# Performance work log

Hardware: AMD Instinct MI355X
Metric: run time of the kernel (lower is better)

The kernel has to match this reference:

```python
import jax, jax.numpy as jnp
import numpy as np

L, H, C, HS, V, BS = 4, 4, 1024, 256, 32000, 1024  # layers, heads, n_embd, head_size, vocab, block_size
B, T = 4, 1024
EPS = 1e-5

def _ln(x, g, b):
    mu = jnp.mean(x, axis=-1, keepdims=True)
    var = jnp.mean((x - mu) ** 2, axis=-1, keepdims=True)
    return (x - mu) / jnp.sqrt(var + EPS) * g + b

def setup_inputs() -> dict:
    key = jax.random.key(0)
    ks = iter(jax.random.split(key, 32))
    s = 0.02
    inp = {
        'idx': jax.random.randint(next(ks), (B, T), 0, V),
        'tok_emb': jax.random.normal(next(ks), (V, C), jnp.float32) * s,
        'pos_emb': jax.random.normal(next(ks), (BS, C), jnp.float32) * s,
        'wq': jax.random.normal(next(ks), (L, H, C, HS), jnp.float32) * s,
        'wk': jax.random.normal(next(ks), (L, H, C, HS), jnp.float32) * s,
        'wv': jax.random.normal(next(ks), (L, H, C, HS), jnp.float32) * s,
        'proj_w': jax.random.normal(next(ks), (L, C, C), jnp.float32) * s,
        'proj_b': jnp.zeros((L, C), jnp.float32),
        'ln1_g': jnp.ones((L, C), jnp.float32),
        'ln1_b': jnp.zeros((L, C), jnp.float32),
        'ln2_g': jnp.ones((L, C), jnp.float32),
        'ln2_b': jnp.zeros((L, C), jnp.float32),
        'ff_w1': jax.random.normal(next(ks), (L, C, 4 * C), jnp.float32) * s,
        'ff_b1': jnp.zeros((L, 4 * C), jnp.float32),
        'ff_w2': jax.random.normal(next(ks), (L, 4 * C, C), jnp.float32) * s,
        'ff_b2': jnp.zeros((L, C), jnp.float32),
        'lnf_g': jnp.ones((C,), jnp.float32),
        'lnf_b': jnp.zeros((C,), jnp.float32),
        'head_w': jax.random.normal(next(ks), (C, V), jnp.float32) * s,
        'head_b': jnp.zeros((V,), jnp.float32),
    }
    return inp

def reference(idx, tok_emb, pos_emb, wq, wk, wv, proj_w, proj_b, ln1_g, ln1_b,
              ln2_g, ln2_b, ff_w1, ff_b1, ff_w2, ff_b2, lnf_g, lnf_b, head_w, head_b):
    b, t = idx.shape
    x = tok_emb[idx] + pos_emb[:t]  # (B,T,C)
    causal = jnp.tril(jnp.ones((t, t), bool))
    inv_sqrt_c = np.float32(1.0 / np.sqrt(C))  # NOTE: original scales by sqrt(n_embd), not head_size
    for l in range(L):
        xn = _ln(x, ln1_g[l], ln1_b[l])
        q = jnp.einsum('btc,hcd->bhtd', xn, wq[l])
        k = jnp.einsum('bsc,hcd->bhsd', xn, wk[l])
        v = jnp.einsum('bsc,hcd->bhsd', xn, wv[l])
        scores = jnp.einsum('bhtd,bhsd->bhts', q, k)
        scores = jnp.where(causal, scores, -jnp.inf) * inv_sqrt_c
        # original: F.softmax(xdot, dim=1) on (B,T,T) -> normalize over the QUERY axis
        alpha = jax.nn.softmax(scores, axis=2)
        y = jnp.einsum('bhts,bhsd->bhtd', alpha, v)
        y = y.transpose(0, 2, 1, 3).reshape(b, t, C)  # concat heads
        x = x + y @ proj_w[l] + proj_b[l]
        xn2 = _ln(x, ln2_g[l], ln2_b[l])
        h = jax.nn.relu(xn2 @ ff_w1[l] + ff_b1[l])
        x = x + h @ ff_w2[l] + ff_b2[l]
    x = _ln(x, lnf_g, lnf_b)
    logits = x @ head_w + head_b  # (B,T,V)
    return logits
```

## Files before the change

### kernel.cpp

```cpp
#include <hip/hip_runtime.h>


#define C_  1024
#define T_  1024
#define HS_ 256
#define H_  4
#define L_  4
#define V_  32000
#define B_  4
#define M_  4096

typedef __attribute__((ext_vector_type(8))) short  bfx8;
typedef __attribute__((ext_vector_type(4))) float  fx4;
typedef __attribute__((ext_vector_type(4))) unsigned short usx4;

__device__ __forceinline__ unsigned short f2bf(float f) {
  unsigned int u = __builtin_bit_cast(unsigned int, f);
  u += 0x7fffu + ((u >> 16) & 1u);
  return (unsigned short)(u >> 16);
}
__device__ __forceinline__ float bf2f(unsigned short u) {
  return __builtin_bit_cast(float, ((unsigned int)u) << 16);
}

__device__ __forceinline__ void gload16(const unsigned short* g, unsigned short* l) {
  __builtin_amdgcn_global_load_lds(
      (const __attribute__((address_space(1))) unsigned int*)g,
      (__attribute__((address_space(3))) unsigned int*)l, 16, 0, 0);
}

template<int BIAS, int RES, int RELU, int OUTBF>
__global__ __launch_bounds__(256, 2) void gemm_bf16(
    const unsigned short* __restrict__ A, const unsigned short* __restrict__ Bm,
    const float* __restrict__ bias, const float* __restrict__ res,
    void* __restrict__ out,
    int M, int N, int K, int lda, int ldb, int ldc,
    long sA, long sB, long sC1, long sC2, int zShift, long rowOuter)
{
  __shared__ unsigned short As[128 * 32];
  __shared__ unsigned short Bs[128 * 32];
  const int z = blockIdx.z;
  A  += (long)z * sA;
  Bm += (long)z * sB;
  const long outOff = ((long)(z >> zShift)) * sC1 + (long)(z & ((1 << zShift) - 1)) * sC2;
  const int m0 = blockIdx.x * 128, n0 = blockIdx.y * 128;
  const int tid = threadIdx.x;
  const int lane = tid & 63, wave = tid >> 6;
  const int wm = (wave >> 1) * 64, wn = (wave & 1) * 64;
  const int fr = lane & 15, kb = lane >> 4;
  const int sr = lane >> 2;
  const int csw = (((lane & 3) ^ ((lane >> 3) & 3)) << 3);
  const int aco = ((kb ^ ((lane >> 1) & 3)) << 3);

  fx4 acc[4][4] = {};

  for (int k0 = 0; k0 < K; k0 += 32) {
    #pragma unroll
    for (int i = 0; i < 2; ++i) {
      const int c = wave * 2 + i;
      gload16(A  + (long)(m0 + c * 16 + sr) * lda + k0 + csw, &As[c * 512]);
      gload16(Bm + (long)(n0 + c * 16 + sr) * ldb + k0 + csw, &Bs[c * 512]);
    }
    __syncthreads();
    bfx8 af[4], bf[4];
    #pragma unroll
    for (int i = 0; i < 4; ++i)
      af[i] = *reinterpret_cast<const bfx8*>(&As[(wm + i * 16 + fr) * 32 + aco]);
    #pragma unroll
    for (int j = 0; j < 4; ++j)
      bf[j] = *reinterpret_cast<const bfx8*>(&Bs[(wn + j * 16 + fr) * 32 + aco]);
    #pragma unroll
    for (int i = 0; i < 4; ++i)
      #pragma unroll
      for (int j = 0; j < 4; ++j)
        acc[i][j] = __builtin_amdgcn_mfma_f32_16x16x32_bf16(af[i], bf[j], acc[i][j], 0, 0, 0);
    __syncthreads();
  }

  const float* resp = res;
  if (RES) resp += outOff;
  const int rbase = (lane >> 4) * 4;
  #pragma unroll
  for (int j = 0; j < 4; ++j) {
    const int n = n0 + wn + j * 16 + fr;
    float bv = 0.f;
    if (BIAS) bv = bias[n];
    #pragma unroll
    for (int i = 0; i < 4; ++i) {
      #pragma unroll
      for (int r = 0; r < 4; ++r) {
        const int m = m0 + wm + i * 16 + rbase + r;
        const long off = outOff + ((long)(m >> 10)) * rowOuter + (long)(m & 1023) * ldc + n;
        float val = acc[i][j][r] + bv;
        if (RELU) val = fmaxf(val, 0.f);
        if (RES) val += resp[((long)(m >> 10)) * rowOuter + (long)(m & 1023) * ldc + n];
        if (OUTBF) ((unsigned short*)out)[off] = f2bf(val);
        else       ((float*)out)[off] = val;
      }
    }
  }
}

#define BAR() __builtin_amdgcn_s_barrier()
#define LGKM() { asm volatile("s_waitcnt lgkmcnt(0)" ::: "memory"); \
                 __builtin_amdgcn_sched_barrier(0); }
#define VM6()  asm volatile("s_waitcnt vmcnt(6)" ::: "memory")
#define RD_A(p, kh, rh) { _Pragma("unroll") for (int i = 0; i < 4; ++i) \
  af[i] = *reinterpret_cast<const bfx8*>(&S[((p)*2+(kh))*8192 + (wr*128 + (rh)*64 + i*16 + fr)*32 + aco]); }
#define RD_B(p, kh) { _Pragma("unroll") for (int j = 0; j < 4; ++j) \
  bf[j] = *reinterpret_cast<const bfx8*>(&S[32768 + ((p)*2+(kh))*8192 + (wc*64 + j*16 + fr)*32 + aco]); }
#define MM16(rh) { __builtin_amdgcn_s_setprio(1); \
  _Pragma("unroll") for (int i = 0; i < 4; ++i) { _Pragma("unroll") for (int j = 0; j < 4; ++j) \
    acc[(rh)*4+i][j] = __builtin_amdgcn_mfma_f32_16x16x32_bf16(af[i], bf[j], acc[(rh)*4+i][j], 0, 0, 0); } \
  __builtin_amdgcn_s_setprio(0); }

template<int BIAS, int RELU, int OUTBF, int EPI>
__global__ __launch_bounds__(512, 2) void gemm256(
    const unsigned short* __restrict__ A, const unsigned short* __restrict__ Bm,
    const float* __restrict__ bias, void* __restrict__ out,
    int K, int lda, int ldb, int ldc,
    long sA, long sB, long sC1, long rowOuter)
{
  __shared__ unsigned short S[65536];
  const int z = blockIdx.z;
  A  += (long)z * sA;
  Bm += (long)z * sB;
  const long outOff = (long)z * sC1;
  const int m0 = blockIdx.x * 256, n0 = blockIdx.y * 256;
  const int tid = threadIdx.x;
  const int lane = tid & 63, wave = tid >> 6;
  const int wr = wave >> 2, wc = wave & 3;
  const int fr = lane & 15, kb = lane >> 4;
  const int srow = lane >> 2;
  const int csw = (((lane & 3) ^ ((lane >> 2) & 3)) << 3);
  const int aco = ((kb ^ (fr & 3)) << 3);
  const int NT = K >> 6;
  const int NI = NT >> 1;

  fx4 acc[8][4] = {};
  bfx8 af[4], bf[4];

  auto stA = [&](int tau, int kh) {
    const int tc = tau < NT ? tau : NT - 1;
    const unsigned short* src = A + (long)(m0 + wave * 16 + srow) * lda + tc * 64 + kh * 32 + csw;
    unsigned short* d = &S[((tau & 1) * 2 + kh) * 8192 + wave * 512];
    gload16(src, d);
    gload16(src + (long)128 * lda, d + 4096);
  };
  auto stB = [&](int tau, int kh) {
    const int tc = tau < NT ? tau : NT - 1;
    const unsigned short* src = Bm + (long)(n0 + wave * 16 + srow) * ldb + tc * 64 + kh * 32 + csw;
    unsigned short* d = &S[32768 + ((tau & 1) * 2 + kh) * 8192 + wave * 512];
    gload16(src, d);
    gload16(src + (long)128 * ldb, d + 4096);
  };

  stA(0, 0); stB(0, 0); stA(0, 1); stB(0, 1); stA(1, 0); stB(1, 0);
  asm volatile("s_waitcnt vmcnt(8)" ::: "memory");
  BAR();

  for (int t = 0; t < NI; ++t) {
    const int u = 2 * t;
    RD_A(0, 0, 0); RD_B(0, 0); stA(u + 1, 1);
    BAR(); LGKM(); MM16(0); BAR();
    RD_A(0, 0, 1); stB(u + 1, 1);
    BAR(); LGKM(); MM16(1); VM6(); BAR();
    RD_A(0, 1, 0); RD_B(0, 1); stA(u + 2, 0);
    BAR(); LGKM(); MM16(0); BAR();
    RD_A(0, 1, 1); stB(u + 2, 0);
    BAR(); LGKM(); MM16(1); VM6(); BAR();
    RD_A(1, 0, 0); RD_B(1, 0); stA(u + 2, 1);
    BAR(); LGKM(); MM16(0); BAR();
    RD_A(1, 0, 1); stB(u + 2, 1);
    BAR(); LGKM(); MM16(1); VM6(); BAR();
    RD_A(1, 1, 0); RD_B(1, 1); stA(u + 3, 0);
    BAR(); LGKM(); MM16(0); BAR();
    RD_A(1, 1, 1); stB(u + 3, 0);
    BAR(); LGKM(); MM16(1); VM6(); BAR();
  }
  asm volatile("s_waitcnt vmcnt(0)" ::: "memory");

  const int rbase = (lane >> 4) * 4;
  if (EPI == 1) {
    const int sel = n0 >> 10, h = (n0 >> 8) & 3;
    unsigned short* dst = (unsigned short*)out
        + (long)sel * ((long)B_ * H_ * T_ * HS_) + (long)h * T_ * HS_;
    #pragma unroll
    for (int j = 0; j < 4; ++j) {
      const int d = wc * 64 + j * 16 + fr;
      #pragma unroll
      for (int i = 0; i < 8; ++i) {
        #pragma unroll
        for (int r = 0; r < 4; ++r) {
          const int m = m0 + wr * 128 + i * 16 + rbase + r;
          const int bq = m >> 10, tq = m & 1023;
          dst[(long)bq * H_ * T_ * HS_ + (long)tq * HS_ + d] = f2bf(acc[i][j][r]);
        }
      }
    }
  } else {
    #pragma unroll
    for (int j = 0; j < 4; ++j) {
      const int n = n0 + wc * 64 + j * 16 + fr;
      float bv = 0.f;
      if (BIAS) bv = bias[n];
      #pragma unroll
      for (int i = 0; i < 8; ++i) {
        #pragma unroll
        for (int r = 0; r < 4; ++r) {
          const int m = m0 + wr * 128 + i * 16 + rbase + r;
          const long off = outOff + ((long)(m >> 10)) * rowOuter + (long)(m & 1023) * ldc + n;
          float val = acc[i][j][r] + bv;
          if (RELU) val = fmaxf(val, 0.f);
          if (OUTBF) ((unsigned short*)out)[off] = f2bf(val);
          else       ((float*)out)[off] = val;
        }
      }
    }
  }
}

template<typename TIN>
__global__ __launch_bounds__(256) void transpose_k(const TIN* __restrict__ src,
    unsigned short* __restrict__ dst, int R, int Cc, int zShiftT, long sOuter) {
  __shared__ float ts[64][65];
  const long zb = blockIdx.z;
  src += zb * (long)R * Cc;
  dst += (zb >> zShiftT) * sOuter + (zb & ((1 << zShiftT) - 1)) * ((long)R * Cc);
  const int r0 = blockIdx.y * 64, c0 = blockIdx.x * 64;
  const int tr = threadIdx.x >> 4;
  const int tc = (threadIdx.x & 15) * 4;
  #pragma unroll
  for (int it = 0; it < 4; ++it) {
    const int r = tr + it * 16;
    float4 v;
    if constexpr (sizeof(TIN) == 4) {
      v = *reinterpret_cast<const float4*>(src + (long)(r0 + r) * Cc + c0 + tc);
    } else {
      usx4 u = *reinterpret_cast<const usx4*>(src + (long)(r0 + r) * Cc + c0 + tc);
      v.x = bf2f(u[0]); v.y = bf2f(u[1]); v.z = bf2f(u[2]); v.w = bf2f(u[3]);
    }
    ts[r][tc + 0] = v.x; ts[r][tc + 1] = v.y; ts[r][tc + 2] = v.z; ts[r][tc + 3] = v.w;
  }
  __syncthreads();
  #pragma unroll
  for (int it = 0; it < 4; ++it) {
    const int cj = tr + it * 16;
    usx4 o = { f2bf(ts[tc + 0][cj]), f2bf(ts[tc + 1][cj]),
               f2bf(ts[tc + 2][cj]), f2bf(ts[tc + 3][cj]) };
    *reinterpret_cast<usx4*>(dst + (long)(c0 + cj) * R + r0 + tc) = o;
  }
}

__global__ __launch_bounds__(256) void embed_k(const int* __restrict__ idx,
                                               const float* __restrict__ tok,
                                               const float* __restrict__ pos,
                                               float* __restrict__ x) {
  const int row = blockIdx.x;
  const int t = row & (T_ - 1);
  const int id = idx[row];
  const int c = threadIdx.x * 4;
  const float4 a = *reinterpret_cast<const float4*>(tok + (long)id * C_ + c);
  const float4 p = *reinterpret_cast<const float4*>(pos + (long)t * C_ + c);
  float4 ov = { a.x + p.x, a.y + p.y, a.z + p.z, a.w + p.w };
  *reinterpret_cast<float4*>(x + (long)row * C_ + c) = ov;
}

__global__ __launch_bounds__(256) void ln_k(const float* __restrict__ x,
                                            const float* __restrict__ g,
                                            const float* __restrict__ b,
                                            unsigned short* __restrict__ o) {
  __shared__ float red[8];
  const int row = blockIdx.x;
  const int c = threadIdx.x * 4;
  const float4 v = *reinterpret_cast<const float4*>(x + (long)row * C_ + c);
  float s1 = v.x + v.y + v.z + v.w;
  float s2 = v.x * v.x + v.y * v.y + v.z * v.z + v.w * v.w;
  #pragma unroll
  for (int off = 32; off; off >>= 1) {
    s1 += __shfl_xor(s1, off, 64);
    s2 += __shfl_xor(s2, off, 64);
  }
  const int lane = threadIdx.x & 63, w = threadIdx.x >> 6;
  if (lane == 0) { red[w] = s1; red[4 + w] = s2; }
  __syncthreads();
  s1 = red[0] + red[1] + red[2] + red[3];
  s2 = red[4] + red[5] + red[6] + red[7];
  const float mu = s1 * (1.f / C_);
  float var = s2 * (1.f / C_) - mu * mu;
  var = fmaxf(var, 0.f);
  const float inv = rsqrtf(var + 1e-5f);
  const float4 gg = *reinterpret_cast<const float4*>(g + c);
  const float4 bb = *reinterpret_cast<const float4*>(b + c);
  usx4 ov;
  ov[0] = f2bf((v.x - mu) * inv * gg.x + bb.x);
  ov[1] = f2bf((v.y - mu) * inv * gg.y + bb.y);
  ov[2] = f2bf((v.z - mu) * inv * gg.z + bb.z);
  ov[3] = f2bf((v.w - mu) * inv * gg.w + bb.w);
  *reinterpret_cast<usx4*>(o + (long)row * C_ + c) = ov;
}

__global__ __launch_bounds__(256) void colsm_k(const unsigned short* __restrict__ a,
                                               unsigned short* __restrict__ aT) {
  __shared__ float red[8];
  const int row = blockIdx.x;
  const int s = row & (T_ - 1);
  const unsigned short* p = a + (long)row * T_;
  const int t0 = threadIdx.x * 4;
  const usx4 u = *reinterpret_cast<const usx4*>(p + t0);
  const float scale = 0.03125f;
  float vals[4];
  float m = -1e30f;
  #pragma unroll
  for (int j = 0; j < 4; ++j) {
    vals[j] = (t0 + j >= s) ? bf2f(u[j]) * scale : -1e30f;
    m = fmaxf(m, vals[j]);
  }
  #pragma unroll
  for (int off = 32; off; off >>= 1) m = fmaxf(m, __shfl_xor(m, off, 64));
  const int lane = threadIdx.x & 63, w = threadIdx.x >> 6;
  if (lane == 0) red[w] = m;
  __syncthreads();
  m = fmaxf(fmaxf(red[0], red[1]), fmaxf(red[2], red[3]));
  __syncthreads();
  float e[4], sum = 0.f;
  #pragma unroll
  for (int j = 0; j < 4; ++j) {
    e[j] = (t0 + j >= s) ? __expf(vals[j] - m) : 0.f;
    sum += e[j];
  }
  #pragma unroll
  for (int off = 32; off; off >>= 1) sum += __shfl_xor(sum, off, 64);
  if (lane == 0) red[w] = sum;
  __syncthreads();
  sum = red[0] + red[1] + red[2] + red[3];
  const float inv = 1.f / sum;
  usx4 ov = { f2bf(e[0] * inv), f2bf(e[1] * inv), f2bf(e[2] * inv), f2bf(e[3] * inv) };
  *reinterpret_cast<usx4*>(aT + (long)row * T_ + t0) = ov;
}

extern "C" void kernel_launch(void* const* d_in, const int* in_sizes, int n_in,
                              void* d_out, int out_size, void* d_ws, size_t ws_size,
                              hipStream_t stream) {
  const int*   idx    = (const int*)d_in[0];
  const float* tok    = (const float*)d_in[1];
  const float* pos    = (const float*)d_in[2];
  const float* wq     = (const float*)d_in[3];
  const float* wk     = (const float*)d_in[4];
  const float* wv     = (const float*)d_in[5];
  const float* proj_w = (const float*)d_in[6];
  const float* proj_b = (const float*)d_in[7];
  const float* ln1_g  = (const float*)d_in[8];
  const float* ln1_b  = (const float*)d_in[9];
  const float* ln2_g  = (const float*)d_in[10];
  const float* ln2_b  = (const float*)d_in[11];
  const float* ff_w1  = (const float*)d_in[12];
  const float* ff_b1  = (const float*)d_in[13];
  const float* ff_w2  = (const float*)d_in[14];
  const float* ff_b2  = (const float*)d_in[15];
  const float* lnf_g  = (const float*)d_in[16];
  const float* lnf_b  = (const float*)d_in[17];
  const float* head_w = (const float*)d_in[18];
  const float* head_b = (const float*)d_in[19];
  float* outp = (float*)d_out;

  typedef unsigned short us;
  char* w = (char*)d_ws;
  float* x    = (float*)(w + 0);
  us* xn      = (us*)(w + 16777216);
  us* qkv     = (us*)(w + 25165824);
  us* kptr    = qkv + 4194304;
  us* vptr    = qkv + 8388608;
  us* vT      = (us*)(w + 50331648);
  us* yc      = (us*)(w + 58720256);
  us* sc      = (us*)(w + 67108864);
  us* headT   = (us*)(w + 67108864);
  us* alpha   = (us*)(w + 100663296);
  us* aT      = (us*)(w + 134217728);
  us* hidden  = aT;
  us* wqkvT   = (us*)(w + 167772160);
  us* projT   = (us*)(w + 192937984);
  us* ff1T    = (us*)(w + 201326592);
  us* ff2T    = (us*)(w + 234881024);
  if (ws_size < (size_t)268435456) return;

  const long HHC = (long)H_ * HS_ * C_;
  transpose_k<float><<<dim3(HS_/64, C_/64, L_*H_), 256, 0, stream>>>(wq, wqkvT,           C_, HS_, 2, 3*HHC);
  transpose_k<float><<<dim3(HS_/64, C_/64, L_*H_), 256, 0, stream>>>(wk, wqkvT + HHC,     C_, HS_, 2, 3*HHC);
  transpose_k<float><<<dim3(HS_/64, C_/64, L_*H_), 256, 0, stream>>>(wv, wqkvT + 2*HHC,   C_, HS_, 2, 3*HHC);
  transpose_k<float><<<dim3(C_/64, C_/64, L_), 256, 0, stream>>>(proj_w, projT, C_, C_, 0, (long)C_*C_);
  transpose_k<float><<<dim3(4*C_/64, C_/64, L_), 256, 0, stream>>>(ff_w1, ff1T, C_, 4*C_, 0, (long)C_*4*C_);
  transpose_k<float><<<dim3(C_/64, 4*C_/64, L_), 256, 0, stream>>>(ff_w2, ff2T, 4*C_, C_, 0, (long)4*C_*C_);

  embed_k<<<M_, 256, 0, stream>>>(idx, tok, pos, x);

  for (int l = 0; l < L_; ++l) {
    ln_k<<<M_, 256, 0, stream>>>(x, ln1_g + l * C_, ln1_b + l * C_, xn);

    dim3 gqkv(M_/256, 3*C_/256, 1);
    gemm256<0,0,1,1><<<gqkv, 512, 0, stream>>>(xn, wqkvT + l * 3 * HHC, nullptr, qkv,
        C_, C_, C_, 0, 0, 0, 0, 0);

    dim3 gs(T_/256, T_/256, B_*H_);
    gemm256<0,0,1,0><<<gs, 512, 0, stream>>>(kptr, qkv, nullptr, sc,
        HS_, HS_, HS_, T_, (long)T_*HS_, (long)T_*HS_, (long)T_*T_, 0);

    colsm_k<<<B_*H_*T_, 256, 0, stream>>>(sc, aT);

    transpose_k<us><<<dim3(T_/64, T_/64, B_*H_), 256, 0, stream>>>(aT, alpha, T_, T_, 0, (long)T_*T_);
    transpose_k<us><<<dim3(HS_/64, T_/64, B_*H_), 256, 0, stream>>>(vptr, vT, T_, HS_, 0, (long)T_*HS_);

    dim3 gp(T_/128, HS_/128, B_*H_);
    gemm_bf16<0,0,0,1><<<gp, 256, 0, stream>>>(alpha, vT, nullptr, nullptr, yc,
        T_, HS_, T_, T_, T_, C_, (long)T_*T_, (long)HS_*T_, (long)T_*C_, HS_, 2, (long)T_*C_);

    dim3 gj(M_/128, C_/128, 1);
    gemm_bf16<1,1,0,0><<<gj, 256, 0, stream>>>(yc, projT + (long)l*C_*C_, proj_b + l*C_, x, x,
        M_, C_, C_, C_, C_, C_, 0, 0, 0, 0, 0, (long)T_*C_);

    ln_k<<<M_, 256, 0, stream>>>(x, ln2_g + l * C_, ln2_b + l * C_, xn);

    dim3 g1(M_/256, 4*C_/256, 1);
    gemm256<1,1,1,0><<<g1, 512, 0, stream>>>(xn, ff1T + (long)l*4*C_*C_, ff_b1 + (long)l*4*C_,
        hidden, C_, C_, C_, 4*C_, 0, 0, 0, (long)1024*4*C_);

    dim3 g2(M_/128, C_/128, 1);
    gemm_bf16<1,1,0,0><<<g2, 256, 0, stream>>>(hidden, ff2T + (long)l*C_*4*C_, ff_b2 + l*C_, x, x,
        M_, C_, 4*C_, 4*C_, 4*C_, C_, 0, 0, 0, 0, 0, (long)T_*C_);
  }

  ln_k<<<M_, 256, 0, stream>>>(x, lnf_g, lnf_b, xn);

  transpose_k<float><<<dim3(V_/64, C_/64, 1), 256, 0, stream>>>(head_w, headT, C_, V_, 0, (long)C_*V_);

  dim3 gh(M_/256, V_/256, 1);
  gemm256<1,0,0,0><<<gh, 512, 0, stream>>>(xn, headT, head_b, outp,
      C_, C_, C_, V_, 0, 0, 0, (long)1024*V_);
}
```

Baseline: 1.715 ms.

## Stage GEMM epilogue through LDS for vectorized coalesced stores; change LDS swizzle

The non-QKV GEMM epilogue now writes each wave's accumulator tile into shared memory with an XOR swizzle. It then reads rows back as float4 vectors, so bias add, ReLU, bf16 conversion and global stores happen in 4-wide coalesced chunks instead of scattered scalar stores. The operand-load swizzle pattern (csw/aco) is also changed, which is intended to cut LDS bank conflicts. A barrier is added before the epilogue because the shared buffer is reused, and the epilogue now spends extra LDS traffic and instructions.

```diff
diff --git a/kernel.cpp b/kernel.cpp
--- a/kernel.cpp
+++ b/kernel.cpp
@@ -132,8 +132,8 @@
   const int wr = wave >> 2, wc = wave & 3;
   const int fr = lane & 15, kb = lane >> 4;
   const int srow = lane >> 2;
-  const int csw = (((lane & 3) ^ ((lane >> 2) & 3)) << 3);
-  const int aco = ((kb ^ (fr & 3)) << 3);
+  const int csw = (((lane & 3) ^ (((lane >> 5) & 1) << 1)) << 3);
+  const int aco = ((kb ^ (((fr >> 3) & 1) << 1)) << 3);
   const int NT = K >> 6;
   const int NI = NT >> 1;
 
@@ -179,6 +179,7 @@
     BAR(); LGKM(); MM16(1); VM6(); BAR();
   }
   asm volatile("s_waitcnt vmcnt(0)" ::: "memory");
+  BAR();
 
   const int rbase = (lane >> 4) * 4;
   if (EPI == 1) {
@@ -199,23 +200,44 @@
       }
     }
   } else {
-    #pragma unroll
-    for (int j = 0; j < 4; ++j) {
-      const int n = n0 + wc * 64 + j * 16 + fr;
-      float bv = 0.f;
-      if (BIAS) bv = bias[n];
+    float* lf = (float*)S;
+    #pragma unroll
+    for (int jh = 0; jh < 2; ++jh) {
       #pragma unroll
-      for (int i = 0; i < 8; ++i) {
+      for (int jj = 0; jj < 2; ++jj)
         #pragma unroll
-        for (int r = 0; r < 4; ++r) {
-          const int m = m0 + wr * 128 + i * 16 + rbase + r;
-          const long off = outOff + ((long)(m >> 10)) * rowOuter + (long)(m & 1023) * ldc + n;
-          float val = acc[i][j][r] + bv;
-          if (RELU) val = fmaxf(val, 0.f);
-          if (OUTBF) ((unsigned short*)out)[off] = f2bf(val);
-          else       ((float*)out)[off] = val;
+        for (int i = 0; i < 8; ++i)
+          #pragma unroll
+          for (int r = 0; r < 4; ++r) {
+            const int row = i * 16 + rbase + r;
+            const int cw = (jj * 16 + fr) ^ ((row & 7) << 2);
+            lf[wave * 4096 + row * 32 + cw] = acc[i][jh * 2 + jj][r];
+          }
+      #pragma unroll
+      for (int rs = 0; rs < 16; ++rs) {
+        const int row = rs * 8 + (lane >> 3);
+        const int c0 = (lane & 7) * 4;
+        const int cw = c0 ^ ((row & 7) << 2);
+        fx4 val = *reinterpret_cast<const fx4*>(&lf[wave * 4096 + row * 32 + cw]);
+        const int n = n0 + wc * 64 + jh * 32 + c0;
+        const int m = m0 + wr * 128 + row;
+        const long off = outOff + ((long)(m >> 10)) * rowOuter + (long)(m & 1023) * ldc + n;
+        if (BIAS) {
+          const float4 bb = *reinterpret_cast<const float4*>(bias + n);
+          val[0] += bb.x; val[1] += bb.y; val[2] += bb.z; val[3] += bb.w;
+        }
+        if (RELU) {
+          val[0] = fmaxf(val[0], 0.f); val[1] = fmaxf(val[1], 0.f);
+          val[2] = fmaxf(val[2], 0.f); val[3] = fmaxf(val[3], 0.f);
+        }
+        if (OUTBF) {
+          usx4 o = { f2bf(val[0]), f2bf(val[1]), f2bf(val[2]), f2bf(val[3]) };
+          *reinterpret_cast<usx4*>((unsigned short*)out + off) = o;
+        } else {
+          *reinterpret_cast<float4*>((float*)out + off) = *(const float4*)&val;
         }
       }
+      __builtin_amdgcn_sched_barrier(0);
     }
   }
 }
```

Result: faster. 1.610 ms (-6.1%).
